# Kernel tuning notes

Hardware: AMD Instinct MI355X
Metric: run time of the kernel (lower is better)

The kernel has to match this reference:

```python
import jax, jax.numpy as jnp
import numpy as np
from jax import lax

SAMPLE_RATE = 44100.0


def _biquad(x, b0, b1, b2, a1, a2):
    """Direct-form-I biquad over last axis. x: [B,C,S]; coefs: [B,1] (broadcast over C).
    y[n] = b0*x[n] + b1*x[n-1] + b2*x[n-2] - a1*y[n-1] - a2*y[n-2], zero initial state
    (identical to torchaudio.functional.biquad)."""

    def step(carry, xn):  # xn: [B,C]
        x1, x2, y1, y2 = carry
        y = b0 * xn + b1 * x1 + b2 * x2 - a1 * y1 - a2 * y2
        return (xn, x1, y, y1), y

    xs = jnp.moveaxis(x, -1, 0)  # [S,B,C]
    z = jnp.zeros_like(x[..., 0])
    _, ys = lax.scan(step, (z, z, z, z), xs)
    return jnp.moveaxis(ys, 0, -1)  # [B,C,S]


def _peaking_coeffs(freq, gain, q):
    """RBJ peaking EQ coefficients, normalized by a0. Inputs: [B] -> outputs [B,1]."""
    w0 = 2.0 * jnp.pi * freq / SAMPLE_RATE
    alpha = jnp.sin(w0) / (2.0 * q)
    A = jnp.power(10.0, gain / 40.0)
    cosw0 = jnp.cos(w0)
    b0 = 1.0 + alpha * A
    b1 = -2.0 * cosw0
    b2 = 1.0 - alpha * A
    a0 = 1.0 + alpha / A
    a1 = -2.0 * cosw0
    a2 = 1.0 - alpha / A
    coefs = (b0 / a0, b1 / a0, b2 / a0, a1 / a0, a2 / a0)
    return tuple(c[:, None] for c in coefs)  # broadcast over channel dim


def setup_inputs() -> dict:
    key = jax.random.key(0)
    k1, k2, k3, k4 = jax.random.split(key, 4)
    B, C, S, NB = 32, 2, 262144, 10
    audio = jax.random.normal(k1, (B, C, S), dtype=jnp.float32)
    center_freqs = jax.random.uniform(k2, (B, NB), dtype=jnp.float32, minval=100.0, maxval=10000.0)
    gains = jax.random.uniform(k3, (B, NB), dtype=jnp.float32, minval=-12.0, maxval=12.0)
    q_factors = jax.random.uniform(k4, (B, NB), dtype=jnp.float32, minval=0.5, maxval=4.0)
    return {"audio": audio, "center_freqs": center_freqs, "gains": gains, "q_factors": q_factors}


def reference(audio, center_freqs, gains, q_factors):
    num_bands = center_freqs.shape[1]
    out = audio
    for band in range(num_bands):  # fixed small cascade of structurally distinct filters
        b0, b1, b2, a1, a2 = _peaking_coeffs(center_freqs[:, band], gains[:, band], q_factors[:, band])
        out = _biquad(out, b0, b1, b2, a1, a2)
    return out
```

## Files before the change

kernel.cpp:

```cpp
#include <hip/hip_runtime.h>


#define B_   32
#define C_   2
#define S_   262144
#define NB   10
#define SEQ  64

#define F_LCH   64
#define F_PCH   4096
#define F_G     8
#define F_GRP   512
#define F_NPOW  11

#define F_OFF_POW 1600
#define F_OFF_T   142400
#define F_OFF_G   5385280
#define F_OFF_SB  6040640
#define F_TOT     6696000

__global__ __launch_bounds__(256) void setup_kernel(
    const float* __restrict__ freqs, const float* __restrict__ gains,
    const float* __restrict__ qs, float* __restrict__ coef,
    float* __restrict__ powers) {
  __shared__ float bufA[400], bufB[400];
  __shared__ float cfs[NB * 5];
  const int b = blockIdx.x, tid = threadIdx.x;
  for (int e = tid; e < 400; e += 256) bufA[e] = 0.0f;
  if (tid < NB) {
    int idx = b * NB + tid;
    float f = freqs[idx], g = gains[idx], Q = qs[idx];
    float w0 = 6.28318530717958648f * f / 44100.0f;
    float sw = sinf(w0), cw = cosf(w0);
    float alpha = sw / (2.0f * Q);
    float A = expf(g * 0.05756462732485114f);
    float aA = alpha * A, adA = alpha / A;
    float inv = 1.0f / (1.0f + adA);
    float c0 = (1.0f + aA) * inv;
    float c1 = -2.0f * cw * inv;
    float c2 = (1.0f - aA) * inv;
    float c3 = 2.0f * cw * inv;
    float c4 = -(1.0f - adA) * inv;
    cfs[tid*5+0] = c0; cfs[tid*5+1] = c1; cfs[tid*5+2] = c2;
    cfs[tid*5+3] = c3; cfs[tid*5+4] = c4;
    float* o = coef + idx * 5;
    o[0] = c0; o[1] = c1; o[2] = c2; o[3] = c3; o[4] = c4;
  }
  __syncthreads();
  if (tid < 20) {
    int c = tid;
    float rp = 0.0f;
    for (int k = 0; k < NB; k++) {
      float b0 = cfs[k*5+0], b1 = cfs[k*5+1], b2 = cfs[k*5+2];
      float na1 = cfs[k*5+3], na2 = cfs[k*5+4];
      float val = (k > 0) ? b0 * rp : 0.0f;
      if (k > 0) {
        if (c == 2*k-2) val += b1;
        if (c == 2*k-1) val += b2;
      }
      if (c == 2*k)   val += na1;
      if (c == 2*k+1) val += na2;
      bufA[2*k*20 + c] = val;
      rp = val;
      if (c == 2*k) bufA[(2*k+1)*20 + c] = 1.0f;
    }
  }
  __syncthreads();
  float* cur = bufA;
  float* nxt = bufB;
  float* pw = powers + (size_t)b * F_NPOW * 400;
  for (int j = 1; j <= 17; j++) {
    for (int e = tid; e < 400; e += 256) {
      int r = e / 20, c = e % 20;
      float acc = 0.0f;
      #pragma unroll
      for (int k = 0; k < 20; k++) acc = fmaf(cur[r*20+k], cur[k*20+c], acc);
      nxt[e] = acc;
    }
    __syncthreads();
    { float* t_ = cur; cur = nxt; nxt = t_; }
    int slot = -1;
    if (j == 6) slot = 0;
    else if (j == 8) slot = 1;
    else if (j == 9) slot = 2;
    else if (j >= 10) slot = j - 7;
    if (slot >= 0) for (int e = tid; e < 400; e += 256) pw[slot*400 + e] = cur[e];
  }
}

template <bool WRITE_OUT>
__global__ __launch_bounds__(64) void pass_v3(
    const float* __restrict__ x, const float* __restrict__ coef,
    const float* __restrict__ tst, float* __restrict__ tout,
    float* __restrict__ out) {
  __shared__ float4 lds4[1024];
  const int seq = blockIdx.y;
  const int b = seq >> 1;
  const int lane = threadIdx.x;
  const int wgc0 = blockIdx.x * 64;
  const int chunk = wgc0 + lane;
  const float* cf = coef + b * NB * 5;
  float b0[NB], b1[NB], b2[NB], na1[NB], na2[NB];
  #pragma unroll
  for (int k = 0; k < NB; k++) {
    b0[k] = cf[k*5+0]; b1[k] = cf[k*5+1]; b2[k] = cf[k*5+2];
    na1[k] = cf[k*5+3]; na2[k] = cf[k*5+4];
  }
  const size_t span0 = (size_t)seq * S_ + (size_t)wgc0 * F_LCH;
  const float4* gx = (const float4*)(x + span0);
  #pragma unroll 4
  for (int it = 0; it < 16; it++) {
    int f = it * 64 + lane;
    float4 v = gx[f];
    int c = f >> 4, q = f & 15;
    lds4[c*16 + (q ^ (c & 15))] = v;
  }
  __syncthreads();
  float x1 = 0.0f, x2 = 0.0f;
  if (lane == 0) {
    if (chunk > 0) {
      const float* xs = x + span0;
      x1 = xs[-1]; x2 = xs[-2];
    }
  } else {
    float4 pv = lds4[(lane-1)*16 + (15 ^ ((lane-1) & 15))];
    x2 = pv.z; x1 = pv.w;
  }
  float p[NB], q_[NB];
  if (WRITE_OUT && chunk > 0) {
    const float4* sv = (const float4*)(tst + ((size_t)seq * F_PCH + chunk - 1) * 20);
    #pragma unroll
    for (int i = 0; i < 5; i++) {
      float4 a = sv[i];
      p[2*i] = a.x; q_[2*i] = a.y; p[2*i+1] = a.z; q_[2*i+1] = a.w;
    }
  } else {
    #pragma unroll
    for (int k = 0; k < NB; k++) { p[k] = 0.0f; q_[k] = 0.0f; }
  }
  #pragma unroll 2
  for (int qq = 0; qq < 16; qq++) {
    const int slot = lane*16 + (qq ^ (lane & 15));
    float4 xv = lds4[slot];
    float xin[4] = {xv.x, xv.y, xv.z, xv.w};
    float o[4];
    #pragma unroll
    for (int j = 0; j < 4; j++) {
      float u = xin[j], u1 = x1, u2 = x2;
      x2 = x1; x1 = xin[j];
      #pragma unroll
      for (int k = 0; k < NB; k++) {
        float v = fmaf(b0[k], u,
                  fmaf(b1[k], u1,
                  fmaf(b2[k], u2,
                  fmaf(na1[k], p[k], na2[k] * q_[k]))));
        u1 = p[k]; u2 = q_[k];
        q_[k] = p[k]; p[k] = v;
        u = v;
      }
      o[j] = u;
    }
    if (WRITE_OUT) lds4[slot] = make_float4(o[0], o[1], o[2], o[3]);
  }
  if (WRITE_OUT) {
    __syncthreads();
    float4* gy = (float4*)(out + span0);
    #pragma unroll 4
    for (int it = 0; it < 16; it++) {
      int f = it * 64 + lane;
      int c = f >> 4, q = f & 15;
      gy[f] = lds4[c*16 + (q ^ (c & 15))];
    }
  } else {
    float4* td = (float4*)(tout + ((size_t)seq * F_PCH + chunk) * 20);
    #pragma unroll
    for (int i = 0; i < 5; i++)
      td[i] = make_float4(p[2*i], q_[2*i], p[2*i+1], q_[2*i+1]);
  }
}

template <bool WRITE_BACK>
__global__ __launch_bounds__(256) void scan_horner(
    float* __restrict__ t, const float* __restrict__ powers,
    float* __restrict__ gbuf, const float* __restrict__ sbuf) {
  __shared__ float Msh[400];
  const int seq = blockIdx.y, b = seq >> 1;
  const int g = blockIdx.x * 256 + threadIdx.x;
  const float* pw0 = powers + (size_t)b * F_NPOW * 400;
  for (int e = threadIdx.x; e < 400; e += 256) {
    int r = e / 20, c = e % 20;
    Msh[c*20 + r] = pw0[e];
  }
  __syncthreads();
  float s[20];
  if (WRITE_BACK) {
    const float4* sv = (const float4*)(sbuf + ((size_t)seq * F_GRP + g) * 20);
    #pragma unroll
    for (int i = 0; i < 5; i++) {
      float4 a = sv[i];
      s[4*i] = a.x; s[4*i+1] = a.y; s[4*i+2] = a.z; s[4*i+3] = a.w;
    }
  } else {
    #pragma unroll
    for (int r = 0; r < 20; r++) s[r] = 0.0f;
  }
  float* tp = t + ((size_t)seq * F_PCH + (size_t)g * F_G) * 20;
  const float4* tv = (const float4*)tp;
  float4 nx[5];
  #pragma unroll
  for (int i = 0; i < 5; i++) nx[i] = tv[i];
  #pragma unroll 1
  for (int j = 0; j < F_G; j++) {
    float ns[20];
    #pragma unroll
    for (int i = 0; i < 5; i++) {
      float4 a = nx[i];
      ns[4*i] = a.x; ns[4*i+1] = a.y; ns[4*i+2] = a.z; ns[4*i+3] = a.w;
    }
    if (j < F_G - 1) {
      #pragma unroll
      for (int i = 0; i < 5; i++) nx[i] = tv[(j+1)*5 + i];
    }
    #pragma unroll
    for (int c = 0; c < 20; c++) {
      float vc = s[c];
      const float4* col = (const float4*)&Msh[c*20];
      float4 c0 = col[0], c1 = col[1], c2 = col[2], c3 = col[3], c4 = col[4];
      ns[0]  = fmaf(c0.x, vc, ns[0]);  ns[1]  = fmaf(c0.y, vc, ns[1]);
      ns[2]  = fmaf(c0.z, vc, ns[2]);  ns[3]  = fmaf(c0.w, vc, ns[3]);
      ns[4]  = fmaf(c1.x, vc, ns[4]);  ns[5]  = fmaf(c1.y, vc, ns[5]);
      ns[6]  = fmaf(c1.z, vc, ns[6]);  ns[7]  = fmaf(c1.w, vc, ns[7]);
      ns[8]  = fmaf(c2.x, vc, ns[8]);  ns[9]  = fmaf(c2.y, vc, ns[9]);
      ns[10] = fmaf(c2.z, vc, ns[10]); ns[11] = fmaf(c2.w, vc, ns[11]);
      ns[12] = fmaf(c3.x, vc, ns[12]); ns[13] = fmaf(c3.y, vc, ns[13]);
      ns[14] = fmaf(c3.z, vc, ns[14]); ns[15] = fmaf(c3.w, vc, ns[15]);
      ns[16] = fmaf(c4.x, vc, ns[16]); ns[17] = fmaf(c4.y, vc, ns[17]);
      ns[18] = fmaf(c4.z, vc, ns[18]); ns[19] = fmaf(c4.w, vc, ns[19]);
    }
    #pragma unroll
    for (int r = 0; r < 20; r++) s[r] = ns[r];
    if (WRITE_BACK) {
      float4* tw = (float4*)(tp + j * 20);
      #pragma unroll
      for (int i = 0; i < 5; i++)
        tw[i] = make_float4(s[4*i], s[4*i+1], s[4*i+2], s[4*i+3]);
    }
  }
  if (!WRITE_BACK) {
    float4* gw = (float4*)(gbuf + ((size_t)seq * F_GRP + g) * 20);
    #pragma unroll
    for (int i = 0; i < 5; i++)
      gw[i] = make_float4(s[4*i], s[4*i+1], s[4*i+2], s[4*i+3]);
  }
}

__global__ __launch_bounds__(512) void scan_ks(
    const float* __restrict__ gbuf, const float* __restrict__ powers,
    float* __restrict__ sbuf) {
  __shared__ float h[F_GRP * 20];
  __shared__ float Ksh[400];
  const int seq = blockIdx.x, b = seq >> 1, i = threadIdx.x;
  const float* pw = powers + (size_t)b * F_NPOW * 400;
  float own[20];
  {
    const float4* gv = (const float4*)(gbuf + ((size_t)seq * F_GRP + i) * 20);
    #pragma unroll
    for (int k = 0; k < 5; k++) {
      float4 a = gv[k];
      own[4*k] = a.x; own[4*k+1] = a.y; own[4*k+2] = a.z; own[4*k+3] = a.w;
    }
  }
  #pragma unroll
  for (int r = 0; r < 20; r++) h[i*20 + r] = own[r];
  for (int s = 0; s < 9; s++) {
    const int d = 1 << s;
    const float* pwS = pw + (size_t)(2 + s) * 400;
    __syncthreads();
    for (int e = i; e < 400; e += 512) {
      int r = e / 20, c = e % 20;
      Ksh[c*20 + r] = pwS[e];
    }
    float nb[20];
    if (i >= d) {
      const float4* hv = (const float4*)&h[(i - d) * 20];
      #pragma unroll
      for (int k = 0; k < 5; k++) {
        float4 a = hv[k];
        nb[4*k] = a.x; nb[4*k+1] = a.y; nb[4*k+2] = a.z; nb[4*k+3] = a.w;
      }
    }
    __syncthreads();
    if (i >= d) {
      #pragma unroll
      for (int c = 0; c < 20; c++) {
        float vc = nb[c];
        const float4* col = (const float4*)&Ksh[c*20];
        float4 c0 = col[0], c1 = col[1], c2 = col[2], c3 = col[3], c4 = col[4];
        own[0]  = fmaf(c0.x, vc, own[0]);  own[1]  = fmaf(c0.y, vc, own[1]);
        own[2]  = fmaf(c0.z, vc, own[2]);  own[3]  = fmaf(c0.w, vc, own[3]);
        own[4]  = fmaf(c1.x, vc, own[4]);  own[5]  = fmaf(c1.y, vc, own[5]);
        own[6]  = fmaf(c1.z, vc, own[6]);  own[7]  = fmaf(c1.w, vc, own[7]);
        own[8]  = fmaf(c2.x, vc, own[8]);  own[9]  = fmaf(c2.y, vc, own[9]);
        own[10] = fmaf(c2.z, vc, own[10]); own[11] = fmaf(c2.w, vc, own[11]);
        own[12] = fmaf(c3.x, vc, own[12]); own[13] = fmaf(c3.y, vc, own[13]);
        own[14] = fmaf(c3.z, vc, own[14]); own[15] = fmaf(c3.w, vc, own[15]);
        own[16] = fmaf(c4.x, vc, own[16]); own[17] = fmaf(c4.y, vc, own[17]);
        own[18] = fmaf(c4.z, vc, own[18]); own[19] = fmaf(c4.w, vc, own[19]);
      }
      #pragma unroll
      for (int r = 0; r < 20; r++) h[i*20 + r] = own[r];
    }
  }
  __syncthreads();
  float4* sw = (float4*)(sbuf + ((size_t)seq * F_GRP + i) * 20);
  if (i > 0) {
    const float4* hv = (const float4*)&h[(i - 1) * 20];
    #pragma unroll
    for (int k = 0; k < 5; k++) sw[k] = hv[k];
  } else {
    #pragma unroll
    for (int k = 0; k < 5; k++) sw[k] = make_float4(0.f, 0.f, 0.f, 0.f);
  }
}

extern "C" void kernel_launch(void* const* d_in, const int* in_sizes, int n_in,
                              void* d_out, int out_size, void* d_ws, size_t ws_size,
                              hipStream_t stream) {
  const float* audio = (const float*)d_in[0];
  const float* freqs = (const float*)d_in[1];
  const float* gains = (const float*)d_in[2];
  const float* qs    = (const float*)d_in[3];
  float* out = (float*)d_out;
  float* ws  = (float*)d_ws;
  float* coef   = ws;
  float* powers = ws + F_OFF_POW;
  float* t      = ws + F_OFF_T;
  float* gbuf   = ws + F_OFF_G;
  float* sbuf   = ws + F_OFF_SB;

  hipLaunchKernelGGL(setup_kernel, dim3(B_), dim3(256), 0, stream,
                     freqs, gains, qs, coef, powers);
  hipLaunchKernelGGL((pass_v3<false>), dim3(F_PCH / 64, SEQ), dim3(64), 0, stream,
                     audio, coef, (const float*)nullptr, t, (float*)nullptr);
  hipLaunchKernelGGL((scan_horner<false>), dim3(F_GRP / 256, SEQ), dim3(256),
                     0, stream, t, powers, gbuf, (const float*)nullptr);
  hipLaunchKernelGGL(scan_ks, dim3(SEQ), dim3(512), 0, stream,
                     gbuf, powers, sbuf);
  hipLaunchKernelGGL((scan_horner<true>), dim3(F_GRP / 256, SEQ), dim3(256),
                     0, stream, t, powers, (float*)nullptr, sbuf);
  hipLaunchKernelGGL((pass_v3<true>), dim3(F_PCH / 64, SEQ), dim3(64), 0, stream,
                     audio, coef, t, (float*)nullptr, out);
}
```

Baseline: 236.1 us.

## Fuse three scan kernels into one and double-buffer tiles in pass kernel

Merges the two Horner passes and the Kogge-Stone carry scan into a single per-sequence kernel, so the group-carry buffers no longer round-trip through global memory and two launches disappear. The pass kernel now walks four tiles per workgroup, prefetching the next tile into a second LDS buffer with global_load_lds while computing the current one, and also prefetches that tile's edge samples and incoming states. This gives 4x fewer workgroups in the pass kernels (1024 instead of 4096), which risks lower occupancy and less latency hiding. The fused scan runs only 64 workgroups of 512 threads.

```diff
diff --git a/kernel.cpp b/kernel.cpp
--- a/kernel.cpp
+++ b/kernel.cpp
@@ -12,11 +12,10 @@
 #define F_G     8
 #define F_GRP   512
 #define F_NPOW  11
+#define NT      4
 
 #define F_OFF_POW 1600
 #define F_OFF_T   142400
-#define F_OFF_G   5385280
-#define F_OFF_SB  6040640
 #define F_TOT     6696000
 
 __global__ __launch_bounds__(256) void setup_kernel(
@@ -88,17 +87,50 @@
   }
 }
 
+__device__ __forceinline__ void stage_tile(const float* xseq, float4* dst,
+                                           int tile, int lane) {
+  const float4* gx = (const float4*)(xseq + (size_t)tile * 4096);
+  #pragma unroll
+  for (int it = 0; it < 16; it++) {
+    const int f = it * 64 + lane;
+    const int c = f >> 4;
+    const int gi = (c << 4) | ((f & 15) ^ (c & 15));
+    __builtin_amdgcn_global_load_lds(
+        (const __attribute__((address_space(1))) void*)(gx + gi),
+        (__attribute__((address_space(3))) void*)(dst + it * 64),
+        16, 0, 0);
+  }
+}
+
 template <bool WRITE_OUT>
-__global__ __launch_bounds__(64) void pass_v3(
+__device__ __forceinline__ void prefetch_es(
+    const float* xseq, const float* tst, int seq, int tile, int lane,
+    float2& pe, float4 (&pst)[5]) {
+  if (tile > 0) {
+    const float2* ep = (const float2*)(xseq + (size_t)tile * 4096) - 1;
+    pe = *ep;
+  } else {
+    pe = make_float2(0.f, 0.f);
+  }
+  if constexpr (WRITE_OUT) {
+    const int chunk = tile * F_LCH + lane;
+    const int cm1 = chunk > 0 ? chunk - 1 : 0;
+    const float4* sv = (const float4*)(tst + ((size_t)seq * F_PCH + cm1) * 20);
+    #pragma unroll
+    for (int i = 0; i < 5; i++) pst[i] = sv[i];
+  }
+}
+
+template <bool WRITE_OUT>
+__global__ __launch_bounds__(64) void pass_v4(
     const float* __restrict__ x, const float* __restrict__ coef,
     const float* __restrict__ tst, float* __restrict__ tout,
     float* __restrict__ out) {
-  __shared__ float4 lds4[1024];
+  __shared__ float4 lds4[2048];
   const int seq = blockIdx.y;
   const int b = seq >> 1;
   const int lane = threadIdx.x;
-  const int wgc0 = blockIdx.x * 64;
-  const int chunk = wgc0 + lane;
+  const int tile0 = blockIdx.x * NT;
   const float* cf = coef + b * NB * 5;
   float b0[NB], b1[NB], b2[NB], na1[NB], na2[NB];
   #pragma unroll
@@ -106,104 +138,126 @@
     b0[k] = cf[k*5+0]; b1[k] = cf[k*5+1]; b2[k] = cf[k*5+2];
     na1[k] = cf[k*5+3]; na2[k] = cf[k*5+4];
   }
-  const size_t span0 = (size_t)seq * S_ + (size_t)wgc0 * F_LCH;
-  const float4* gx = (const float4*)(x + span0);
-  #pragma unroll 4
-  for (int it = 0; it < 16; it++) {
-    int f = it * 64 + lane;
-    float4 v = gx[f];
-    int c = f >> 4, q = f & 15;
-    lds4[c*16 + (q ^ (c & 15))] = v;
-  }
-  __syncthreads();
-  float x1 = 0.0f, x2 = 0.0f;
-  if (lane == 0) {
-    if (chunk > 0) {
-      const float* xs = x + span0;
-      x1 = xs[-1]; x2 = xs[-2];
-    }
-  } else {
-    float4 pv = lds4[(lane-1)*16 + (15 ^ ((lane-1) & 15))];
-    x2 = pv.z; x1 = pv.w;
-  }
-  float p[NB], q_[NB];
-  if (WRITE_OUT && chunk > 0) {
-    const float4* sv = (const float4*)(tst + ((size_t)seq * F_PCH + chunk - 1) * 20);
-    #pragma unroll
-    for (int i = 0; i < 5; i++) {
-      float4 a = sv[i];
-      p[2*i] = a.x; q_[2*i] = a.y; p[2*i+1] = a.z; q_[2*i+1] = a.w;
-    }
-  } else {
-    #pragma unroll
-    for (int k = 0; k < NB; k++) { p[k] = 0.0f; q_[k] = 0.0f; }
-  }
-  #pragma unroll 2
-  for (int qq = 0; qq < 16; qq++) {
-    const int slot = lane*16 + (qq ^ (lane & 15));
-    float4 xv = lds4[slot];
-    float xin[4] = {xv.x, xv.y, xv.z, xv.w};
-    float o[4];
-    #pragma unroll
-    for (int j = 0; j < 4; j++) {
-      float u = xin[j], u1 = x1, u2 = x2;
-      x2 = x1; x1 = xin[j];
-      #pragma unroll
-      for (int k = 0; k < NB; k++) {
-        float v = fmaf(b0[k], u,
-                  fmaf(b1[k], u1,
-                  fmaf(b2[k], u2,
-                  fmaf(na1[k], p[k], na2[k] * q_[k]))));
-        u1 = p[k]; u2 = q_[k];
-        q_[k] = p[k]; p[k] = v;
-        u = v;
-      }
-      o[j] = u;
-    }
-    if (WRITE_OUT) lds4[slot] = make_float4(o[0], o[1], o[2], o[3]);
-  }
-  if (WRITE_OUT) {
-    __syncthreads();
-    float4* gy = (float4*)(out + span0);
-    #pragma unroll 4
-    for (int it = 0; it < 16; it++) {
-      int f = it * 64 + lane;
-      int c = f >> 4, q = f & 15;
-      gy[f] = lds4[c*16 + (q ^ (c & 15))];
-    }
-  } else {
-    float4* td = (float4*)(tout + ((size_t)seq * F_PCH + chunk) * 20);
-    #pragma unroll
-    for (int i = 0; i < 5; i++)
-      td[i] = make_float4(p[2*i], q_[2*i], p[2*i+1], q_[2*i+1]);
-  }
-}
-
-template <bool WRITE_BACK>
-__global__ __launch_bounds__(256) void scan_horner(
-    float* __restrict__ t, const float* __restrict__ powers,
-    float* __restrict__ gbuf, const float* __restrict__ sbuf) {
+  const float* xseq = x + (size_t)seq * S_;
+
+  float2 peC = make_float2(0.f, 0.f), peN = make_float2(0.f, 0.f);
+  float4 pstC[5] = {}, pstN[5] = {};
+
+  stage_tile(xseq, lds4, tile0, lane);
+  prefetch_es<WRITE_OUT>(xseq, tst, seq, tile0, lane, peC, pstC);
+
+  #pragma unroll 1
+  for (int t = 0; t < NT; t++) {
+    const int tile = tile0 + t;
+    float4* lbuf = lds4 + ((t & 1) << 10);
+    asm volatile("s_waitcnt vmcnt(0) lgkmcnt(0)" ::: "memory");
+    __builtin_amdgcn_sched_barrier(0);
+    if (t + 1 < NT) {
+      stage_tile(xseq, lds4 + (((t + 1) & 1) << 10), tile + 1, lane);
+      prefetch_es<WRITE_OUT>(xseq, tst, seq, tile + 1, lane, peN, pstN);
+    }
+    const int chunk = tile * F_LCH + lane;
+    float x1, x2;
+    if (lane == 0) {
+      x1 = peC.y; x2 = peC.x;
+    } else {
+      float4 pv = lbuf[(lane-1)*16 + (15 ^ ((lane-1) & 15))];
+      x2 = pv.z; x1 = pv.w;
+    }
+    float p[NB], q_[NB];
+    if (WRITE_OUT) {
+      const bool z = (chunk == 0);
+      #pragma unroll
+      for (int i = 0; i < 5; i++) {
+        float4 a = pstC[i];
+        p[2*i]   = z ? 0.f : a.x;  q_[2*i]   = z ? 0.f : a.y;
+        p[2*i+1] = z ? 0.f : a.z;  q_[2*i+1] = z ? 0.f : a.w;
+      }
+    } else {
+      #pragma unroll
+      for (int k = 0; k < NB; k++) { p[k] = 0.0f; q_[k] = 0.0f; }
+    }
+    #pragma unroll 2
+    for (int qq = 0; qq < 16; qq++) {
+      const int slot = lane*16 + (qq ^ (lane & 15));
+      float4 xv = lbuf[slot];
+      float xin[4] = {xv.x, xv.y, xv.z, xv.w};
+      float o[4];
+      #pragma unroll
+      for (int j = 0; j < 4; j++) {
+        float u = xin[j], u1 = x1, u2 = x2;
+        x2 = x1; x1 = xin[j];
+        #pragma unroll
+        for (int k = 0; k < NB; k++) {
+          float v = fmaf(b0[k], u,
+                    fmaf(b1[k], u1,
+                    fmaf(b2[k], u2,
+                    fmaf(na1[k], p[k], na2[k] * q_[k]))));
+          u1 = p[k]; u2 = q_[k];
+          q_[k] = p[k]; p[k] = v;
+          u = v;
+        }
+        o[j] = u;
+      }
+      if (WRITE_OUT) lbuf[slot] = make_float4(o[0], o[1], o[2], o[3]);
+    }
+    if (WRITE_OUT) {
+      asm volatile("" ::: "memory");
+      float4* gy = (float4*)(out + (size_t)seq * S_ + (size_t)tile * 4096);
+      #pragma unroll 4
+      for (int it = 0; it < 16; it++) {
+        int f = it * 64 + lane;
+        int c = f >> 4, q = f & 15;
+        gy[f] = lbuf[c*16 + (q ^ (c & 15))];
+      }
+    } else {
+      float4* td = (float4*)(tout + ((size_t)seq * F_PCH + chunk) * 20);
+      #pragma unroll
+      for (int i = 0; i < 5; i++)
+        td[i] = make_float4(p[2*i], q_[2*i], p[2*i+1], q_[2*i+1]);
+    }
+    peC = peN;
+    #pragma unroll
+    for (int i = 0; i < 5; i++) pstC[i] = pstN[i];
+  }
+}
+
+__device__ __forceinline__ void matvec_acc(const float* M ,
+                                           const float* v, float* acc) {
+  #pragma unroll
+  for (int c = 0; c < 20; c++) {
+    float vc = v[c];
+    const float4* col = (const float4*)&M[c*20];
+    float4 c0 = col[0], c1 = col[1], c2 = col[2], c3 = col[3], c4 = col[4];
+    acc[0]  = fmaf(c0.x, vc, acc[0]);  acc[1]  = fmaf(c0.y, vc, acc[1]);
+    acc[2]  = fmaf(c0.z, vc, acc[2]);  acc[3]  = fmaf(c0.w, vc, acc[3]);
+    acc[4]  = fmaf(c1.x, vc, acc[4]);  acc[5]  = fmaf(c1.y, vc, acc[5]);
+    acc[6]  = fmaf(c1.z, vc, acc[6]);  acc[7]  = fmaf(c1.w, vc, acc[7]);
+    acc[8]  = fmaf(c2.x, vc, acc[8]);  acc[9]  = fmaf(c2.y, vc, acc[9]);
+    acc[10] = fmaf(c2.z, vc, acc[10]); acc[11] = fmaf(c2.w, vc, acc[11]);
+    acc[12] = fmaf(c3.x, vc, acc[12]); acc[13] = fmaf(c3.y, vc, acc[13]);
+    acc[14] = fmaf(c3.z, vc, acc[14]); acc[15] = fmaf(c3.w, vc, acc[15]);
+    acc[16] = fmaf(c4.x, vc, acc[16]); acc[17] = fmaf(c4.y, vc, acc[17]);
+    acc[18] = fmaf(c4.z, vc, acc[18]); acc[19] = fmaf(c4.w, vc, acc[19]);
+  }
+}
+
+__global__ __launch_bounds__(512) void scan_fused(
+    float* __restrict__ t, const float* __restrict__ powers) {
+  __shared__ float h[F_GRP * 20];
   __shared__ float Msh[400];
-  const int seq = blockIdx.y, b = seq >> 1;
-  const int g = blockIdx.x * 256 + threadIdx.x;
+  __shared__ float Ksh[400];
+  const int seq = blockIdx.x, b = seq >> 1;
+  const int g = threadIdx.x;
   const float* pw0 = powers + (size_t)b * F_NPOW * 400;
-  for (int e = threadIdx.x; e < 400; e += 256) {
+  for (int e = g; e < 400; e += 512) {
     int r = e / 20, c = e % 20;
     Msh[c*20 + r] = pw0[e];
   }
   __syncthreads();
   float s[20];
-  if (WRITE_BACK) {
-    const float4* sv = (const float4*)(sbuf + ((size_t)seq * F_GRP + g) * 20);
-    #pragma unroll
-    for (int i = 0; i < 5; i++) {
-      float4 a = sv[i];
-      s[4*i] = a.x; s[4*i+1] = a.y; s[4*i+2] = a.z; s[4*i+3] = a.w;
-    }
-  } else {
-    #pragma unroll
-    for (int r = 0; r < 20; r++) s[r] = 0.0f;
-  }
+  #pragma unroll
+  for (int r = 0; r < 20; r++) s[r] = 0.0f;
   float* tp = t + ((size_t)seq * F_PCH + (size_t)g * F_G) * 20;
   const float4* tv = (const float4*)tp;
   float4 nx[5];
@@ -221,68 +275,23 @@
       #pragma unroll
       for (int i = 0; i < 5; i++) nx[i] = tv[(j+1)*5 + i];
     }
-    #pragma unroll
-    for (int c = 0; c < 20; c++) {
-      float vc = s[c];
-      const float4* col = (const float4*)&Msh[c*20];
-      float4 c0 = col[0], c1 = col[1], c2 = col[2], c3 = col[3], c4 = col[4];
-      ns[0]  = fmaf(c0.x, vc, ns[0]);  ns[1]  = fmaf(c0.y, vc, ns[1]);
-      ns[2]  = fmaf(c0.z, vc, ns[2]);  ns[3]  = fmaf(c0.w, vc, ns[3]);
-      ns[4]  = fmaf(c1.x, vc, ns[4]);  ns[5]  = fmaf(c1.y, vc, ns[5]);
-      ns[6]  = fmaf(c1.z, vc, ns[6]);  ns[7]  = fmaf(c1.w, vc, ns[7]);
-      ns[8]  = fmaf(c2.x, vc, ns[8]);  ns[9]  = fmaf(c2.y, vc, ns[9]);
-      ns[10] = fmaf(c2.z, vc, ns[10]); ns[11] = fmaf(c2.w, vc, ns[11]);
-      ns[12] = fmaf(c3.x, vc, ns[12]); ns[13] = fmaf(c3.y, vc, ns[13]);
-      ns[14] = fmaf(c3.z, vc, ns[14]); ns[15] = fmaf(c3.w, vc, ns[15]);
-      ns[16] = fmaf(c4.x, vc, ns[16]); ns[17] = fmaf(c4.y, vc, ns[17]);
-      ns[18] = fmaf(c4.z, vc, ns[18]); ns[19] = fmaf(c4.w, vc, ns[19]);
-    }
+    matvec_acc(Msh, s, ns);
     #pragma unroll
     for (int r = 0; r < 20; r++) s[r] = ns[r];
-    if (WRITE_BACK) {
-      float4* tw = (float4*)(tp + j * 20);
-      #pragma unroll
-      for (int i = 0; i < 5; i++)
-        tw[i] = make_float4(s[4*i], s[4*i+1], s[4*i+2], s[4*i+3]);
-    }
-  }
-  if (!WRITE_BACK) {
-    float4* gw = (float4*)(gbuf + ((size_t)seq * F_GRP + g) * 20);
-    #pragma unroll
-    for (int i = 0; i < 5; i++)
-      gw[i] = make_float4(s[4*i], s[4*i+1], s[4*i+2], s[4*i+3]);
-  }
-}
-
-__global__ __launch_bounds__(512) void scan_ks(
-    const float* __restrict__ gbuf, const float* __restrict__ powers,
-    float* __restrict__ sbuf) {
-  __shared__ float h[F_GRP * 20];
-  __shared__ float Ksh[400];
-  const int seq = blockIdx.x, b = seq >> 1, i = threadIdx.x;
-  const float* pw = powers + (size_t)b * F_NPOW * 400;
-  float own[20];
-  {
-    const float4* gv = (const float4*)(gbuf + ((size_t)seq * F_GRP + i) * 20);
-    #pragma unroll
-    for (int k = 0; k < 5; k++) {
-      float4 a = gv[k];
-      own[4*k] = a.x; own[4*k+1] = a.y; own[4*k+2] = a.z; own[4*k+3] = a.w;
-    }
-  }
-  #pragma unroll
-  for (int r = 0; r < 20; r++) h[i*20 + r] = own[r];
-  for (int s = 0; s < 9; s++) {
-    const int d = 1 << s;
-    const float* pwS = pw + (size_t)(2 + s) * 400;
+  }
+  #pragma unroll
+  for (int r = 0; r < 20; r++) h[g*20 + r] = s[r];
+  for (int st = 0; st < 9; st++) {
+    const int d = 1 << st;
+    const float* pwS = pw0 + (size_t)(2 + st) * 400;
     __syncthreads();
-    for (int e = i; e < 400; e += 512) {
+    for (int e = g; e < 400; e += 512) {
       int r = e / 20, c = e % 20;
       Ksh[c*20 + r] = pwS[e];
     }
     float nb[20];
-    if (i >= d) {
-      const float4* hv = (const float4*)&h[(i - d) * 20];
+    if (g >= d) {
+      const float4* hv = (const float4*)&h[(g - d) * 20];
       #pragma unroll
       for (int k = 0; k < 5; k++) {
         float4 a = hv[k];
@@ -290,36 +299,48 @@
       }
     }
     __syncthreads();
-    if (i >= d) {
-      #pragma unroll
-      for (int c = 0; c < 20; c++) {
-        float vc = nb[c];
-        const float4* col = (const float4*)&Ksh[c*20];
-        float4 c0 = col[0], c1 = col[1], c2 = col[2], c3 = col[3], c4 = col[4];
-        own[0]  = fmaf(c0.x, vc, own[0]);  own[1]  = fmaf(c0.y, vc, own[1]);
-        own[2]  = fmaf(c0.z, vc, own[2]);  own[3]  = fmaf(c0.w, vc, own[3]);
-        own[4]  = fmaf(c1.x, vc, own[4]);  own[5]  = fmaf(c1.y, vc, own[5]);
-        own[6]  = fmaf(c1.z, vc, own[6]);  own[7]  = fmaf(c1.w, vc, own[7]);
-        own[8]  = fmaf(c2.x, vc, own[8]);  own[9]  = fmaf(c2.y, vc, own[9]);
-        own[10] = fmaf(c2.z, vc, own[10]); own[11] = fmaf(c2.w, vc, own[11]);
-        own[12] = fmaf(c3.x, vc, own[12]); own[13] = fmaf(c3.y, vc, own[13]);
-        own[14] = fmaf(c3.z, vc, own[14]); own[15] = fmaf(c3.w, vc, own[15]);
-        own[16] = fmaf(c4.x, vc, own[16]); own[17] = fmaf(c4.y, vc, own[17]);
-        own[18] = fmaf(c4.z, vc, own[18]); own[19] = fmaf(c4.w, vc, own[19]);
-      }
-      #pragma unroll
-      for (int r = 0; r < 20; r++) h[i*20 + r] = own[r];
+    if (g >= d) {
+      matvec_acc(Ksh, nb, s);
+      #pragma unroll
+      for (int r = 0; r < 20; r++) h[g*20 + r] = s[r];
     }
   }
   __syncthreads();
-  float4* sw = (float4*)(sbuf + ((size_t)seq * F_GRP + i) * 20);
-  if (i > 0) {
-    const float4* hv = (const float4*)&h[(i - 1) * 20];
-    #pragma unroll
-    for (int k = 0; k < 5; k++) sw[k] = hv[k];
+  float sx[20];
+  if (g > 0) {
+    const float4* hv = (const float4*)&h[(g - 1) * 20];
+    #pragma unroll
+    for (int k = 0; k < 5; k++) {
+      float4 a = hv[k];
+      sx[4*k] = a.x; sx[4*k+1] = a.y; sx[4*k+2] = a.z; sx[4*k+3] = a.w;
+    }
   } else {
     #pragma unroll
-    for (int k = 0; k < 5; k++) sw[k] = make_float4(0.f, 0.f, 0.f, 0.f);
+    for (int r = 0; r < 20; r++) sx[r] = 0.0f;
+  }
+  #pragma unroll
+  for (int i = 0; i < 5; i++) nx[i] = tv[i];
+  #pragma unroll
+  for (int r = 0; r < 20; r++) s[r] = sx[r];
+  #pragma unroll 1
+  for (int j = 0; j < F_G; j++) {
+    float ns[20];
+    #pragma unroll
+    for (int i = 0; i < 5; i++) {
+      float4 a = nx[i];
+      ns[4*i] = a.x; ns[4*i+1] = a.y; ns[4*i+2] = a.z; ns[4*i+3] = a.w;
+    }
+    if (j < F_G - 1) {
+      #pragma unroll
+      for (int i = 0; i < 5; i++) nx[i] = tv[(j+1)*5 + i];
+    }
+    matvec_acc(Msh, s, ns);
+    #pragma unroll
+    for (int r = 0; r < 20; r++) s[r] = ns[r];
+    float4* tw = (float4*)(tp + j * 20);
+    #pragma unroll
+    for (int i = 0; i < 5; i++)
+      tw[i] = make_float4(s[4*i], s[4*i+1], s[4*i+2], s[4*i+3]);
   }
 }
 
@@ -335,19 +356,13 @@
   float* coef   = ws;
   float* powers = ws + F_OFF_POW;
   float* t      = ws + F_OFF_T;
-  float* gbuf   = ws + F_OFF_G;
-  float* sbuf   = ws + F_OFF_SB;
 
   hipLaunchKernelGGL(setup_kernel, dim3(B_), dim3(256), 0, stream,
                      freqs, gains, qs, coef, powers);
-  hipLaunchKernelGGL((pass_v3<false>), dim3(F_PCH / 64, SEQ), dim3(64), 0, stream,
+  hipLaunchKernelGGL((pass_v4<false>), dim3(64 / NT, SEQ), dim3(64), 0, stream,
                      audio, coef, (const float*)nullptr, t, (float*)nullptr);
-  hipLaunchKernelGGL((scan_horner<false>), dim3(F_GRP / 256, SEQ), dim3(256),
-                     0, stream, t, powers, gbuf, (const float*)nullptr);
-  hipLaunchKernelGGL(scan_ks, dim3(SEQ), dim3(512), 0, stream,
-                     gbuf, powers, sbuf);
-  hipLaunchKernelGGL((scan_horner<true>), dim3(F_GRP / 256, SEQ), dim3(256),
-                     0, stream, t, powers, (float*)nullptr, sbuf);
-  hipLaunchKernelGGL((pass_v3<true>), dim3(F_PCH / 64, SEQ), dim3(64), 0, stream,
+  hipLaunchKernelGGL(scan_fused, dim3(SEQ), dim3(512), 0, stream,
+                     t, powers);
+  hipLaunchKernelGGL((pass_v4<true>), dim3(64 / NT, SEQ), dim3(64), 0, stream,
                      audio, coef, t, (float*)nullptr, out);
 }
```

After: 520.6 us. 120% more time.
